# Kernel optimization log

Hardware: AMD Instinct MI355X
Metric: run time of the kernel (lower is better)

The kernel has to match this reference:

```python
import jax, jax.numpy as jnp
import numpy as np

N_NODES = 50000
N_EDGES = 800000
NFEAT, NHID, NCLASS = 512, 128, 40
BN_EPS = 1e-5


def setup_inputs() -> dict:
    key = jax.random.key(0)
    ks = jax.random.split(key, 12)
    x = jax.random.normal(ks[0], (N_NODES, NFEAT), dtype=jnp.float32)
    edge_index = jax.random.randint(ks[1], (2, N_EDGES), 0, N_NODES, dtype=jnp.int64)
    edge_weight = jax.random.uniform(ks[2], (N_EDGES,), dtype=jnp.float32)
    def glorot(k, fi, fo):
        lim = (6.0 / (fi + fo)) ** 0.5
        return jax.random.uniform(k, (fi, fo), minval=-lim, maxval=lim, dtype=jnp.float32)
    return {
        "x": x, "edge_index": edge_index, "edge_weight": edge_weight,
        "W1": glorot(ks[3], NFEAT, NHID), "b1": jnp.zeros((NHID,), jnp.float32),
        "W2": glorot(ks[4], NHID, NHID), "b2": jnp.zeros((NHID,), jnp.float32),
        "W3": glorot(ks[5], NHID, NHID), "b3": jnp.zeros((NHID,), jnp.float32),
        "g1": jnp.ones((NHID,), jnp.float32), "be1": jnp.zeros((NHID,), jnp.float32),
        "g2": jnp.ones((NHID,), jnp.float32), "be2": jnp.zeros((NHID,), jnp.float32),
        "g3": jnp.ones((NHID,), jnp.float32), "be3": jnp.zeros((NHID,), jnp.float32),
        "linW": glorot(ks[6], NHID, NCLASS), "linb": jnp.zeros((NCLASS,), jnp.float32),
    }


def _gcn_norm(edge_index, edge_weight, n):
    # PyG gcn_norm: add self-loops (weight 1), symmetric D^-1/2 (A+I) D^-1/2
    loop = jnp.arange(n, dtype=edge_index.dtype)
    row = jnp.concatenate([edge_index[0], loop])
    col = jnp.concatenate([edge_index[1], loop])
    ew = jnp.concatenate([edge_weight, jnp.ones((n,), edge_weight.dtype)])
    deg = jax.ops.segment_sum(ew, col, num_segments=n)
    dinv = jnp.where(deg > 0, jax.lax.rsqrt(jnp.maximum(deg, 1e-30)), 0.0)
    norm = dinv[row] * ew * dinv[col]
    return row, col, norm


def _conv(x, W, b, row, col, norm, n):
    h = x @ W                                   # [N, out]
    msg = h[row] * norm[:, None]                # gather + weight, [E+N, out]
    return jax.ops.segment_sum(msg, col, num_segments=n) + b


def _bn(x, g, b):
    # training-mode BatchNorm over node dim (biased variance)
    mu = jnp.mean(x, axis=0)
    var = jnp.mean((x - mu) ** 2, axis=0)
    return (x - mu) * jax.lax.rsqrt(var + BN_EPS) * g + b


def reference(x, edge_index, edge_weight, W1, b1, W2, b2, W3, b3,
              g1, be1, g2, be2, g3, be3, linW, linb):
    n = x.shape[0]
    row, col, norm = _gcn_norm(edge_index, edge_weight, n)
    x1 = _bn(jax.nn.relu(_conv(x, W1, b1, row, col, norm, n)), g1, be1)
    x2 = _bn(jax.nn.relu(_conv(x1, W2, b2, row, col, norm, n)), g2, be2)
    x3 = _bn(_conv(x2, W3, b3, row, col, norm, n), g3, be3)
    logits = x3 @ linW + linb
    return (logits, jax.nn.softmax(logits, axis=1), x3)
```

## Files before the change

### kernel.cpp

```cpp
#include <hip/hip_runtime.h>
#include <hip/hip_bf16.h>

#define N_NODES 50000
#define N_EDGES 800000
#define NFEAT 512
#define NHID 128
#define NCLASS 40
#define BN_EPS 1e-5f

typedef __attribute__((ext_vector_type(8))) short short8;
typedef __attribute__((ext_vector_type(4))) float f32x4;

#define GEMM1_BLOCKS ((N_NODES + 127) / 128)
#define EDGE_BLOCKS ((N_EDGES + 255) / 256)
#define SCAN_BLOCKS ((N_NODES + 255) / 256)
#define BN_BLOCKS ((N_NODES + 255) / 256)

__device__ __forceinline__ unsigned short f2b(float f) {
    unsigned int u = __float_as_uint(f);
    u += 0x7fff + ((u >> 16) & 1);
    return (unsigned short)(u >> 16);
}
__device__ __forceinline__ float blo(unsigned int v) {
    return __uint_as_float(v << 16);
}
__device__ __forceinline__ float bhi(unsigned int v) {
    return __uint_as_float(v & 0xffff0000u);
}

__global__ void k_init_node(unsigned long long* __restrict__ degcnt) {
    int i = blockIdx.x * blockDim.x + threadIdx.x;
    if (i < N_NODES) degcnt[i] = 0ULL;
}

__global__ void k_prep_w(const float* __restrict__ W1, const float* __restrict__ W2,
                         const float* __restrict__ W3, unsigned short* __restrict__ W1t,
                         unsigned short* __restrict__ W2t, unsigned short* __restrict__ W3t) {
    int i = blockIdx.x * blockDim.x + threadIdx.x;
    if (i < 65536) {
        int k = i >> 7, n = i & 127;
        W1t[n * 512 + k] = f2b(W1[i]);
    } else if (i < 81920) {
        int j = i - 65536; int k = j >> 7, n = j & 127;
        W2t[n * 128 + k] = f2b(W2[j]);
    } else if (i < 98304) {
        int j = i - 81920; int k = j >> 7, n = j & 127;
        W3t[n * 128 + k] = f2b(W3[j]);
    }
}

__global__ __launch_bounds__(256) void k_fat(
    const float* __restrict__ x, const unsigned short* __restrict__ W1t,
    unsigned short* __restrict__ hbuf,
    const unsigned int* __restrict__ words, const float* __restrict__ ew,
    int* __restrict__ row, int* __restrict__ col,
    unsigned long long* __restrict__ degcnt, int* __restrict__ slot) {
    __shared__ unsigned short As[128][40];
    __shared__ unsigned short Bs[128][40];
    __shared__ int s_any;
    int tid = threadIdx.x;
    if (blockIdx.x < GEMM1_BLOCKS) {
        int m0 = blockIdx.x * 128;
        int srow = tid >> 1;
        int skh = (tid & 1) << 4;
        int wave = tid >> 6, lane = tid & 63;
        int wm = (wave >> 1) * 64, wn = (wave & 1) * 64;
        int l15 = lane & 15, quad = lane >> 4;
        f32x4 acc[4][4] = {};
        bool arow_ok = (m0 + srow) < N_NODES;
        const float* arow_p = x + (size_t)(m0 + srow) * 512 + skh;
        const unsigned short* wrow_p = W1t + (size_t)srow * 512 + skh;
        for (int kt = 0; kt < 512; kt += 32) {
            float v[16];
#pragma unroll
            for (int q = 0; q < 4; q++) {
                float4 t4 = make_float4(0.f, 0.f, 0.f, 0.f);
                if (arow_ok) t4 = *(const float4*)(arow_p + kt + q * 4);
                v[q * 4 + 0] = t4.x; v[q * 4 + 1] = t4.y;
                v[q * 4 + 2] = t4.z; v[q * 4 + 3] = t4.w;
            }
            unsigned int p[8];
#pragma unroll
            for (int q = 0; q < 8; q++)
                p[q] = (unsigned int)f2b(v[2 * q]) | ((unsigned int)f2b(v[2 * q + 1]) << 16);
            uint4 w0 = make_uint4(p[0], p[1], p[2], p[3]);
            uint4 w1 = make_uint4(p[4], p[5], p[6], p[7]);
            uint4 b0 = *(const uint4*)(wrow_p + kt);
            uint4 b1 = *(const uint4*)(wrow_p + kt + 8);
            *(uint4*)&As[srow][skh] = w0;
            *(uint4*)&As[srow][skh + 8] = w1;
            *(uint4*)&Bs[srow][skh] = b0;
            *(uint4*)&Bs[srow][skh + 8] = b1;
            __syncthreads();
            short8 a[4], b[4];
#pragma unroll
            for (int i = 0; i < 4; i++) a[i] = *(const short8*)&As[wm + i * 16 + l15][quad * 8];
#pragma unroll
            for (int j = 0; j < 4; j++) b[j] = *(const short8*)&Bs[wn + j * 16 + l15][quad * 8];
#pragma unroll
            for (int i = 0; i < 4; i++)
#pragma unroll
                for (int j = 0; j < 4; j++)
                    acc[i][j] = __builtin_amdgcn_mfma_f32_16x16x32_bf16(a[i], b[j], acc[i][j], 0, 0, 0);
            __syncthreads();
        }
#pragma unroll
        for (int i = 0; i < 4; i++) {
            int mb = m0 + wm + i * 16 + quad * 4;
#pragma unroll
            for (int r = 0; r < 4; r++) {
                int m = mb + r;
                if (m < N_NODES) {
#pragma unroll
                    for (int j = 0; j < 4; j++)
                        hbuf[(size_t)m * 128 + wn + j * 16 + l15] = f2b(acc[i][j][r]);
                }
            }
        }
    } else {
        if (tid == 0) s_any = 0;
        __syncthreads();
        unsigned int probe = words[2 * tid + 1];
        if (probe != 0) atomicAdd(&s_any, 1);
        __syncthreads();
        int f = (s_any == 0) ? 1 : 0;
        int e = (blockIdx.x - GEMM1_BLOCKS) * 256 + tid;
        if (e < N_EDGES) {
            unsigned int r = f ? words[2 * (size_t)e] : words[e];
            unsigned int c = f ? words[2 * ((size_t)e + N_EDGES)] : words[e + N_EDGES];
            row[e] = (int)r;
            col[e] = (int)c;
            unsigned int q = __float2uint_rn(ew[e] * 8388608.0f);
            unsigned long long old = atomicAdd(&degcnt[c], (1ULL << 32) | (unsigned long long)q);
            slot[e] = (int)(old >> 32);
        }
    }
}

__global__ __launch_bounds__(256) void k_dinv(const unsigned long long* __restrict__ degcnt,
                                              float* __restrict__ dinv,
                                              int* __restrict__ counts,
                                              int* __restrict__ bsum) {
    int i = blockIdx.x * 256 + threadIdx.x;
    int cnt = 0;
    if (i < N_NODES) {
        unsigned long long v = degcnt[i];
        float deg = 1.0f + (float)(unsigned int)(v & 0xffffffffULL) * (1.0f / 8388608.0f);
        dinv[i] = rsqrtf(deg);
        cnt = (int)(v >> 32);
        counts[i] = cnt;
    }
    __shared__ int sh[256];
    sh[threadIdx.x] = cnt;
    __syncthreads();
    for (int ofs = 128; ofs > 0; ofs >>= 1) {
        if (threadIdx.x < ofs) sh[threadIdx.x] += sh[threadIdx.x + ofs];
        __syncthreads();
    }
    if (threadIdx.x == 0) bsum[blockIdx.x] = sh[0];
}

__global__ __launch_bounds__(256) void k_scan2(const int* __restrict__ bsum,
                                               int* __restrict__ bpre,
                                               int* __restrict__ colptr) {
    int t = threadIdx.x;
    int v = (t < SCAN_BLOCKS) ? bsum[t] : 0;
    __shared__ int sh[256];
    sh[t] = v;
    __syncthreads();
    for (int ofs = 1; ofs < 256; ofs <<= 1) {
        int u = (t >= ofs) ? sh[t - ofs] : 0;
        __syncthreads();
        sh[t] += u;
        __syncthreads();
    }
    if (t < SCAN_BLOCKS) bpre[t] = sh[t] - v;
    if (t == SCAN_BLOCKS - 1) colptr[N_NODES] = sh[t];
}

__global__ __launch_bounds__(256) void k_scan3(const int* __restrict__ counts,
                                               const int* __restrict__ bpre,
                                               int* __restrict__ colptr) {
    int t = threadIdx.x;
    int i = blockIdx.x * 256 + t;
    int v = (i < N_NODES) ? counts[i] : 0;
    __shared__ int sh[256];
    sh[t] = v;
    __syncthreads();
    for (int ofs = 1; ofs < 256; ofs <<= 1) {
        int u = (t >= ofs) ? sh[t - ofs] : 0;
        __syncthreads();
        sh[t] += u;
        __syncthreads();
    }
    if (i < N_NODES) colptr[i] = bpre[blockIdx.x] + sh[t] - v;
}

__global__ void k_scatter(const int* __restrict__ row, const int* __restrict__ col,
                          const float* __restrict__ ew, const float* __restrict__ dinv,
                          const int* __restrict__ colptr, const int* __restrict__ slot,
                          int2* __restrict__ ern) {
    int e = blockIdx.x * blockDim.x + threadIdx.x;
    if (e < N_EDGES) {
        int c = col[e], r = row[e];
        int p = colptr[c] + slot[e];
        float nrm = dinv[r] * ew[e] * dinv[c];
        ern[p] = make_int2(r, __float_as_int(nrm));
    }
}

__global__ __launch_bounds__(256) void k_aggregate(
    const unsigned int* __restrict__ hb, const int* __restrict__ colptr,
    const int2* __restrict__ ern, const float* __restrict__ dinv,
    const float* __restrict__ bias, unsigned int* __restrict__ out, int relu,
    float* __restrict__ sums, float* __restrict__ sumsq) {
    if (blockIdx.x == 0) {
        if (threadIdx.x < 128) sums[threadIdx.x] = 0.f;
        else sumsq[threadIdx.x - 128] = 0.f;
    }
    int node = (blockIdx.x * blockDim.x + threadIdx.x) >> 6;
    int lane = threadIdx.x & 63;
    if (node >= N_NODES) return;
    float di = dinv[node];
    float selfw = di * di;
    unsigned int sv = hb[(size_t)node * 64 + lane];
    float a0 = selfw * blo(sv);
    float a1 = selfw * bhi(sv);
    float c0 = 0.f, c1 = 0.f;
    int e = colptr[node], end = colptr[node + 1];
    for (; e + 8 <= end; e += 8) {
        int2 rw[8];
#pragma unroll
        for (int q = 0; q < 8; q++) rw[q] = ern[e + q];
        unsigned int v[8];
#pragma unroll
        for (int q = 0; q < 8; q++) v[q] = hb[(size_t)rw[q].x * 64 + lane];
#pragma unroll
        for (int q = 0; q < 8; q++) {
            float w = __int_as_float(rw[q].y);
            if (q & 1) { c0 += w * blo(v[q]); c1 += w * bhi(v[q]); }
            else       { a0 += w * blo(v[q]); a1 += w * bhi(v[q]); }
        }
    }
    for (; e < end; e++) {
        int2 rw = ern[e];
        float w = __int_as_float(rw.y);
        unsigned int v = hb[(size_t)rw.x * 64 + lane];
        a0 += w * blo(v);
        a1 += w * bhi(v);
    }
    a0 += c0; a1 += c1;
    float2 bv = *(const float2*)&bias[2 * lane];
    a0 += bv.x;
    a1 += bv.y;
    if (relu) { a0 = fmaxf(a0, 0.f); a1 = fmaxf(a1, 0.f); }
    out[(size_t)node * 64 + lane] = (unsigned int)f2b(a0) | ((unsigned int)f2b(a1) << 16);
}

__global__ __launch_bounds__(256) void k_bnstats(const unsigned int* __restrict__ x,
                                                 float* __restrict__ sums,
                                                 float* __restrict__ sumsq) {
    int u = threadIdx.x & 63;
    int strip = threadIdx.x >> 6;
    int r0 = blockIdx.x * 256;
    int rend = min(r0 + 256, N_NODES);
    float sl = 0.f, s2l = 0.f, sh_ = 0.f, s2h = 0.f;
    for (int r = r0 + strip; r < rend; r += 4) {
        unsigned int v = x[(size_t)r * 64 + u];
        float a = blo(v), b = bhi(v);
        sl += a; s2l += a * a;
        sh_ += b; s2h += b * b;
    }
    __shared__ float buf[4][64][4];
    buf[strip][u][0] = sl; buf[strip][u][1] = s2l;
    buf[strip][u][2] = sh_; buf[strip][u][3] = s2h;
    __syncthreads();
    if (strip == 0) {
#pragma unroll
        for (int s = 1; s < 4; s++) {
            sl += buf[s][u][0]; s2l += buf[s][u][1];
            sh_ += buf[s][u][2]; s2h += buf[s][u][3];
        }
        atomicAdd(&sums[2 * u], sl);
        atomicAdd(&sums[2 * u + 1], sh_);
        atomicAdd(&sumsq[2 * u], s2l);
        atomicAdd(&sumsq[2 * u + 1], s2h);
    }
}

__global__ __launch_bounds__(256) void k_gemm_h(
    const unsigned int* __restrict__ Ab, const unsigned short* __restrict__ Wt,
    const float* __restrict__ sums, const float* __restrict__ sumsq,
    const float* __restrict__ g, const float* __restrict__ be,
    unsigned short* __restrict__ Out) {
    __shared__ unsigned short As[128][40];
    __shared__ unsigned short Bs[128][40];
    __shared__ float s_sc[128], s_sh[128];
    int tid = threadIdx.x;
    int m0 = blockIdx.x * 128;
    if (tid < 128) {
        const float invn = 1.0f / (float)N_NODES;
        float mu = sums[tid] * invn;
        float var = sumsq[tid] * invn - mu * mu;
        float iv = rsqrtf(var + BN_EPS);
        float sc = g[tid] * iv;
        s_sc[tid] = sc;
        s_sh[tid] = be[tid] - mu * sc;
    }
    __syncthreads();
    int srow = tid >> 1;
    int skh = (tid & 1) << 4;
    int wave = tid >> 6, lane = tid & 63;
    int wm = (wave >> 1) * 64, wn = (wave & 1) * 64;
    int l15 = lane & 15, quad = lane >> 4;
    f32x4 acc[4][4] = {};
    bool arow_ok = (m0 + srow) < N_NODES;
    const unsigned int* arow_b = Ab + (size_t)(m0 + srow) * 64 + (skh >> 1);
    const unsigned short* wrow_p = Wt + (size_t)srow * 128 + skh;
    for (int kt = 0; kt < 128; kt += 32) {
        uint4 r0 = make_uint4(0, 0, 0, 0), r1 = make_uint4(0, 0, 0, 0);
        if (arow_ok) {
            r0 = *(const uint4*)(arow_b + (kt >> 1));
            r1 = *(const uint4*)(arow_b + (kt >> 1) + 4);
        }
        unsigned int raw[8] = {r0.x, r0.y, r0.z, r0.w, r1.x, r1.y, r1.z, r1.w};
        unsigned int p[8];
#pragma unroll
        for (int q = 0; q < 8; q++) {
            int ch = kt + skh + 2 * q;
            float f0 = blo(raw[q]) * s_sc[ch] + s_sh[ch];
            float f1 = bhi(raw[q]) * s_sc[ch + 1] + s_sh[ch + 1];
            p[q] = (unsigned int)f2b(f0) | ((unsigned int)f2b(f1) << 16);
        }
        uint4 w0 = make_uint4(p[0], p[1], p[2], p[3]);
        uint4 w1 = make_uint4(p[4], p[5], p[6], p[7]);
        uint4 b0 = *(const uint4*)(wrow_p + kt);
        uint4 b1 = *(const uint4*)(wrow_p + kt + 8);
        *(uint4*)&As[srow][skh] = w0;
        *(uint4*)&As[srow][skh + 8] = w1;
        *(uint4*)&Bs[srow][skh] = b0;
        *(uint4*)&Bs[srow][skh + 8] = b1;
        __syncthreads();
        short8 a[4], b[4];
#pragma unroll
        for (int i = 0; i < 4; i++) a[i] = *(const short8*)&As[wm + i * 16 + l15][quad * 8];
#pragma unroll
        for (int j = 0; j < 4; j++) b[j] = *(const short8*)&Bs[wn + j * 16 + l15][quad * 8];
#pragma unroll
        for (int i = 0; i < 4; i++)
#pragma unroll
            for (int j = 0; j < 4; j++)
                acc[i][j] = __builtin_amdgcn_mfma_f32_16x16x32_bf16(a[i], b[j], acc[i][j], 0, 0, 0);
        __syncthreads();
    }
#pragma unroll
    for (int i = 0; i < 4; i++) {
        int mb = m0 + wm + i * 16 + quad * 4;
#pragma unroll
        for (int r = 0; r < 4; r++) {
            int m = mb + r;
            if (m < N_NODES) {
#pragma unroll
                for (int j = 0; j < 4; j++)
                    Out[(size_t)m * 128 + wn + j * 16 + l15] = f2b(acc[i][j][r]);
            }
        }
    }
}

__global__ __launch_bounds__(256) void k_logits(const unsigned int* __restrict__ abuf,
                                                const float* __restrict__ sums,
                                                const float* __restrict__ sumsq,
                                                const float* __restrict__ g,
                                                const float* __restrict__ be,
                                                const float* __restrict__ linW,
                                                const float* __restrict__ linb,
                                                float* __restrict__ logits,
                                                float* __restrict__ probs,
                                                float* __restrict__ x3out) {
    __shared__ float Xs[64][130];
    __shared__ float Ws[128 * 40];
    __shared__ float s_sc[128], s_sh[128];
    int tid = threadIdx.x;
    int m0 = blockIdx.x * 64;
    if (tid < 128) {
        const float invn = 1.0f / (float)N_NODES;
        float mu = sums[tid] * invn;
        float var = sumsq[tid] * invn - mu * mu;
        float iv = rsqrtf(var + BN_EPS);
        float sc = g[tid] * iv;
        s_sc[tid] = sc;
        s_sh[tid] = be[tid] - mu * sc;
    }
    for (int q = tid; q < 1280; q += 256)
        *(float4*)&Ws[q * 4] = *(const float4*)&linW[q * 4];
    __syncthreads();
    for (int q = tid; q < 4096; q += 256) {
        int r = q >> 6, u = q & 63;
        int m = m0 + r;
        float f0 = 0.f, f1 = 0.f;
        if (m < N_NODES) {
            unsigned int v = abuf[(size_t)m * 64 + u];
            f0 = blo(v) * s_sc[2 * u] + s_sh[2 * u];
            f1 = bhi(v) * s_sc[2 * u + 1] + s_sh[2 * u + 1];
            *(float2*)&x3out[(size_t)m * 128 + 2 * u] = make_float2(f0, f1);
        }
        *(float2*)&Xs[r][2 * u] = make_float2(f0, f1);
    }
    __syncthreads();
    int r = tid >> 2;
    int cg = tid & 3;
    int cbase = cg * 10;
    float acc[10] = {};
    for (int k = 0; k < 128; k++) {
        float a = Xs[r][k];
#pragma unroll
        for (int j = 0; j < 10; j++) acc[j] += a * Ws[k * 40 + cbase + j];
    }
#pragma unroll
    for (int j = 0; j < 10; j++) acc[j] += linb[cbase + j];
    float m = acc[0];
#pragma unroll
    for (int j = 1; j < 10; j++) m = fmaxf(m, acc[j]);
    m = fmaxf(m, __shfl_xor(m, 1));
    m = fmaxf(m, __shfl_xor(m, 2));
    float ex[10];
    float s = 0.f;
#pragma unroll
    for (int j = 0; j < 10; j++) { ex[j] = expf(acc[j] - m); s += ex[j]; }
    s += __shfl_xor(s, 1);
    s += __shfl_xor(s, 2);
    float inv = 1.0f / s;
    int mrow = m0 + r;
    if (mrow < N_NODES) {
#pragma unroll
        for (int j = 0; j < 10; j++) {
            logits[(size_t)mrow * 40 + cbase + j] = acc[j];
            probs[(size_t)mrow * 40 + cbase + j] = ex[j] * inv;
        }
    }
}

extern "C" void kernel_launch(void* const* d_in, const int* in_sizes, int n_in,
                              void* d_out, int out_size, void* d_ws, size_t ws_size,
                              hipStream_t stream) {
    const float* x = (const float*)d_in[0];
    const unsigned int* eidx = (const unsigned int*)d_in[1];
    const float* ew = (const float*)d_in[2];
    const float* W1 = (const float*)d_in[3];
    const float* b1 = (const float*)d_in[4];
    const float* W2 = (const float*)d_in[5];
    const float* b2 = (const float*)d_in[6];
    const float* W3 = (const float*)d_in[7];
    const float* b3 = (const float*)d_in[8];
    const float* g1 = (const float*)d_in[9];
    const float* be1 = (const float*)d_in[10];
    const float* g2 = (const float*)d_in[11];
    const float* be2 = (const float*)d_in[12];
    const float* g3 = (const float*)d_in[13];
    const float* be3 = (const float*)d_in[14];
    const float* linW = (const float*)d_in[15];
    const float* linb = (const float*)d_in[16];

    float* out = (float*)d_out;
    float* logits = out;
    float* probs = out + (size_t)N_NODES * NCLASS;
    float* x3out = out + 2 * (size_t)N_NODES * NCLASS;

    char* ws = (char*)d_ws;
    size_t off = 0;
    auto take = [&](size_t bytes) -> char* {
        char* p = ws + off;
        off += (bytes + 255) & ~(size_t)255;
        return p;
    };
    int* row32 = (int*)take((size_t)N_EDGES * 4);
    int* col32 = (int*)take((size_t)N_EDGES * 4);
    int* slot = (int*)take((size_t)N_EDGES * 4);
    int* colptr = (int*)take((size_t)(N_NODES + 1) * 4);
    int* counts = (int*)take((size_t)N_NODES * 4);
    unsigned long long* degcnt = (unsigned long long*)take((size_t)N_NODES * 8);
    int2* ern = (int2*)take((size_t)N_EDGES * 8);
    float* dinv = (float*)take((size_t)N_NODES * 4);
    unsigned short* hbuf = (unsigned short*)take((size_t)N_NODES * NHID * 2);
    unsigned short* abuf = (unsigned short*)take((size_t)N_NODES * NHID * 2);
    unsigned short* W1t = (unsigned short*)take((size_t)512 * 128 * 2);
    unsigned short* W2t = (unsigned short*)take((size_t)128 * 128 * 2);
    unsigned short* W3t = (unsigned short*)take((size_t)128 * 128 * 2);
    float* sums = (float*)take(128 * 4);
    float* sumsq = (float*)take(128 * 4);
    int* bsum = (int*)take((size_t)SCAN_BLOCKS * 4);
    int* bpre = (int*)take((size_t)SCAN_BLOCKS * 4);
    (void)ws_size; (void)n_in; (void)in_sizes; (void)out_size;

    const int TPB = 256;
    int grid_e = EDGE_BLOCKS;
    int grid_gemm = GEMM1_BLOCKS;
    int grid_agg = (N_NODES * 64 + TPB - 1) / TPB;
    int grid_head = (N_NODES + 63) / 64;

    k_init_node<<<SCAN_BLOCKS, TPB, 0, stream>>>(degcnt);
    k_prep_w<<<(98304 + TPB - 1) / TPB, TPB, 0, stream>>>(W1, W2, W3, W1t, W2t, W3t);
    k_fat<<<GEMM1_BLOCKS + EDGE_BLOCKS, TPB, 0, stream>>>(
        x, W1t, hbuf, eidx, ew, row32, col32, degcnt, slot);
    k_dinv<<<SCAN_BLOCKS, TPB, 0, stream>>>(degcnt, dinv, counts, bsum);
    k_scan2<<<1, TPB, 0, stream>>>(bsum, bpre, colptr);
    k_scan3<<<SCAN_BLOCKS, TPB, 0, stream>>>(counts, bpre, colptr);
    k_scatter<<<grid_e, TPB, 0, stream>>>(row32, col32, ew, dinv, colptr, slot, ern);

    k_aggregate<<<grid_agg, TPB, 0, stream>>>((const unsigned int*)hbuf, colptr, ern, dinv, b1, (unsigned int*)abuf, 1, sums, sumsq);
    k_bnstats<<<BN_BLOCKS, TPB, 0, stream>>>((const unsigned int*)abuf, sums, sumsq);

    k_gemm_h<<<grid_gemm, TPB, 0, stream>>>((const unsigned int*)abuf, W2t, sums, sumsq, g1, be1, hbuf);
    k_aggregate<<<grid_agg, TPB, 0, stream>>>((const unsigned int*)hbuf, colptr, ern, dinv, b2, (unsigned int*)abuf, 1, sums, sumsq);
    k_bnstats<<<BN_BLOCKS, TPB, 0, stream>>>((const unsigned int*)abuf, sums, sumsq);

    k_gemm_h<<<grid_gemm, TPB, 0, stream>>>((const unsigned int*)abuf, W3t, sums, sumsq, g2, be2, hbuf);
    k_aggregate<<<grid_agg, TPB, 0, stream>>>((const unsigned int*)hbuf, colptr, ern, dinv, b3, (unsigned int*)abuf, 0, sums, sumsq);
    k_bnstats<<<BN_BLOCKS, TPB, 0, stream>>>((const unsigned int*)abuf, sums, sumsq);

    k_logits<<<grid_head, TPB, 0, stream>>>((const unsigned int*)abuf, sums, sumsq, g3, be3, linW, linb, logits, probs, x3out);
}
```

Before: 494.6 us.

## Spread degree atomics over eight sub-counters and merge scan and prep kernels

Each edge block now adds its atomic degree/count update to one of eight copies per destination node, chosen by block index, to reduce same-address atomic contention. The dinv kernel merges the copies and records per-copy base offsets, which the scatter kernel uses to place edges into CSR slots. The two-level scan is merged into one kernel where every block redoes the block-sum scan, and the init and weight-prep kernels are fused, saving launches. In exchange the degree buffer is eight times larger, zero-initialization writes more memory, and CSR building does more reads.

Result: no change. 499.2 us (+0.9%).

```diff
diff --git a/kernel.cpp b/kernel.cpp
--- a/kernel.cpp
+++ b/kernel.cpp
@@ -15,6 +15,7 @@
 #define EDGE_BLOCKS ((N_EDGES + 255) / 256)
 #define SCAN_BLOCKS ((N_NODES + 255) / 256)
 #define BN_BLOCKS ((N_NODES + 255) / 256)
+#define DEG8 (N_NODES * 8)
 
 __device__ __forceinline__ unsigned short f2b(float f) {
     unsigned int u = __float_as_uint(f);
@@ -28,24 +29,22 @@
     return __uint_as_float(v & 0xffff0000u);
 }
 
-__global__ void k_init_node(unsigned long long* __restrict__ degcnt) {
+__global__ void k_init_prep(unsigned long long* __restrict__ degcnt8,
+                            const float* __restrict__ W1, const float* __restrict__ W2,
+                            const float* __restrict__ W3, unsigned short* __restrict__ W1t,
+                            unsigned short* __restrict__ W2t, unsigned short* __restrict__ W3t) {
     int i = blockIdx.x * blockDim.x + threadIdx.x;
-    if (i < N_NODES) degcnt[i] = 0ULL;
-}
-
-__global__ void k_prep_w(const float* __restrict__ W1, const float* __restrict__ W2,
-                         const float* __restrict__ W3, unsigned short* __restrict__ W1t,
-                         unsigned short* __restrict__ W2t, unsigned short* __restrict__ W3t) {
-    int i = blockIdx.x * blockDim.x + threadIdx.x;
-    if (i < 65536) {
-        int k = i >> 7, n = i & 127;
-        W1t[n * 512 + k] = f2b(W1[i]);
-    } else if (i < 81920) {
-        int j = i - 65536; int k = j >> 7, n = j & 127;
-        W2t[n * 128 + k] = f2b(W2[j]);
-    } else if (i < 98304) {
-        int j = i - 81920; int k = j >> 7, n = j & 127;
-        W3t[n * 128 + k] = f2b(W3[j]);
+    if (i < DEG8) { degcnt8[i] = 0ULL; return; }
+    int j = i - DEG8;
+    if (j < 65536) {
+        int k = j >> 7, n = j & 127;
+        W1t[n * 512 + k] = f2b(W1[j]);
+    } else if (j < 81920) {
+        int q = j - 65536; int k = q >> 7, n = q & 127;
+        W2t[n * 128 + k] = f2b(W2[q]);
+    } else if (j < 98304) {
+        int q = j - 81920; int k = q >> 7, n = q & 127;
+        W3t[n * 128 + k] = f2b(W3[q]);
     }
 }
 
@@ -54,7 +53,7 @@
     unsigned short* __restrict__ hbuf,
     const unsigned int* __restrict__ words, const float* __restrict__ ew,
     int* __restrict__ row, int* __restrict__ col,
-    unsigned long long* __restrict__ degcnt, int* __restrict__ slot) {
+    unsigned long long* __restrict__ degcnt8, int* __restrict__ slot) {
     __shared__ unsigned short As[128][40];
     __shared__ unsigned short Bs[128][40];
     __shared__ int s_any;
@@ -124,31 +123,43 @@
         if (probe != 0) atomicAdd(&s_any, 1);
         __syncthreads();
         int f = (s_any == 0) ? 1 : 0;
-        int e = (blockIdx.x - GEMM1_BLOCKS) * 256 + tid;
+        int eb = blockIdx.x - GEMM1_BLOCKS;
+        int e = eb * 256 + tid;
+        int copy = eb & 7;
         if (e < N_EDGES) {
             unsigned int r = f ? words[2 * (size_t)e] : words[e];
             unsigned int c = f ? words[2 * ((size_t)e + N_EDGES)] : words[e + N_EDGES];
             row[e] = (int)r;
             col[e] = (int)c;
             unsigned int q = __float2uint_rn(ew[e] * 8388608.0f);
-            unsigned long long old = atomicAdd(&degcnt[c], (1ULL << 32) | (unsigned long long)q);
+            unsigned long long old = atomicAdd(&degcnt8[(size_t)c * 8 + copy],
+                                               (1ULL << 32) | (unsigned long long)q);
             slot[e] = (int)(old >> 32);
         }
     }
 }
 
-__global__ __launch_bounds__(256) void k_dinv(const unsigned long long* __restrict__ degcnt,
+__global__ __launch_bounds__(256) void k_dinv(const unsigned long long* __restrict__ degcnt8,
                                               float* __restrict__ dinv,
                                               int* __restrict__ counts,
+                                              int* __restrict__ base8,
                                               int* __restrict__ bsum) {
     int i = blockIdx.x * 256 + threadIdx.x;
     int cnt = 0;
     if (i < N_NODES) {
-        unsigned long long v = degcnt[i];
-        float deg = 1.0f + (float)(unsigned int)(v & 0xffffffffULL) * (1.0f / 8388608.0f);
+        unsigned int fx = 0;
+        int run = 0;
+#pragma unroll
+        for (int c = 0; c < 8; c++) {
+            unsigned long long v = degcnt8[(size_t)i * 8 + c];
+            base8[i * 8 + c] = run;
+            run += (int)(v >> 32);
+            fx += (unsigned int)(v & 0xffffffffULL);
+        }
+        float deg = 1.0f + (float)fx * (1.0f / 8388608.0f);
         dinv[i] = rsqrtf(deg);
-        cnt = (int)(v >> 32);
-        counts[i] = cnt;
+        counts[i] = run;
+        cnt = run;
     }
     __shared__ int sh[256];
     sh[threadIdx.x] = cnt;
@@ -160,12 +171,25 @@
     if (threadIdx.x == 0) bsum[blockIdx.x] = sh[0];
 }
 
-__global__ __launch_bounds__(256) void k_scan2(const int* __restrict__ bsum,
-                                               int* __restrict__ bpre,
-                                               int* __restrict__ colptr) {
+__global__ __launch_bounds__(256) void k_scan(const int* __restrict__ counts,
+                                              const int* __restrict__ bsum,
+                                              int* __restrict__ colptr) {
     int t = threadIdx.x;
-    int v = (t < SCAN_BLOCKS) ? bsum[t] : 0;
+    __shared__ int shb[256];
+    int vb = (t < SCAN_BLOCKS) ? bsum[t] : 0;
+    shb[t] = vb;
+    __syncthreads();
+    for (int ofs = 1; ofs < 256; ofs <<= 1) {
+        int u = (t >= ofs) ? shb[t - ofs] : 0;
+        __syncthreads();
+        shb[t] += u;
+        __syncthreads();
+    }
+    int bpre = (blockIdx.x > 0) ? shb[blockIdx.x - 1] : 0;
+    int total = shb[SCAN_BLOCKS - 1];
     __shared__ int sh[256];
+    int i = blockIdx.x * 256 + t;
+    int v = (i < N_NODES) ? counts[i] : 0;
     sh[t] = v;
     __syncthreads();
     for (int ofs = 1; ofs < 256; ofs <<= 1) {
@@ -174,36 +198,19 @@
         sh[t] += u;
         __syncthreads();
     }
-    if (t < SCAN_BLOCKS) bpre[t] = sh[t] - v;
-    if (t == SCAN_BLOCKS - 1) colptr[N_NODES] = sh[t];
-}
-
-__global__ __launch_bounds__(256) void k_scan3(const int* __restrict__ counts,
-                                               const int* __restrict__ bpre,
-                                               int* __restrict__ colptr) {
-    int t = threadIdx.x;
-    int i = blockIdx.x * 256 + t;
-    int v = (i < N_NODES) ? counts[i] : 0;
-    __shared__ int sh[256];
-    sh[t] = v;
-    __syncthreads();
-    for (int ofs = 1; ofs < 256; ofs <<= 1) {
-        int u = (t >= ofs) ? sh[t - ofs] : 0;
-        __syncthreads();
-        sh[t] += u;
-        __syncthreads();
-    }
-    if (i < N_NODES) colptr[i] = bpre[blockIdx.x] + sh[t] - v;
+    if (i < N_NODES) colptr[i] = bpre + sh[t] - v;
+    if (blockIdx.x == 0 && t == 0) colptr[N_NODES] = total;
 }
 
 __global__ void k_scatter(const int* __restrict__ row, const int* __restrict__ col,
                           const float* __restrict__ ew, const float* __restrict__ dinv,
-                          const int* __restrict__ colptr, const int* __restrict__ slot,
-                          int2* __restrict__ ern) {
+                          const int* __restrict__ colptr, const int* __restrict__ base8,
+                          const int* __restrict__ slot, int2* __restrict__ ern) {
     int e = blockIdx.x * blockDim.x + threadIdx.x;
     if (e < N_EDGES) {
         int c = col[e], r = row[e];
-        int p = colptr[c] + slot[e];
+        int copy = (e >> 8) & 7;
+        int p = colptr[c] + base8[c * 8 + copy] + slot[e];
         float nrm = dinv[r] * ew[e] * dinv[c];
         ern[p] = make_int2(r, __float_as_int(nrm));
     }
@@ -479,7 +486,8 @@
     int* slot = (int*)take((size_t)N_EDGES * 4);
     int* colptr = (int*)take((size_t)(N_NODES + 1) * 4);
     int* counts = (int*)take((size_t)N_NODES * 4);
-    unsigned long long* degcnt = (unsigned long long*)take((size_t)N_NODES * 8);
+    unsigned long long* degcnt8 = (unsigned long long*)take((size_t)DEG8 * 8);
+    int* base8 = (int*)take((size_t)DEG8 * 4);
     int2* ern = (int2*)take((size_t)N_EDGES * 8);
     float* dinv = (float*)take((size_t)N_NODES * 4);
     unsigned short* hbuf = (unsigned short*)take((size_t)N_NODES * NHID * 2);
@@ -490,23 +498,20 @@
     float* sums = (float*)take(128 * 4);
     float* sumsq = (float*)take(128 * 4);
     int* bsum = (int*)take((size_t)SCAN_BLOCKS * 4);
-    int* bpre = (int*)take((size_t)SCAN_BLOCKS * 4);
     (void)ws_size; (void)n_in; (void)in_sizes; (void)out_size;
 
     const int TPB = 256;
-    int grid_e = EDGE_BLOCKS;
+    int grid_initprep = (DEG8 + 98304 + TPB - 1) / TPB;
     int grid_gemm = GEMM1_BLOCKS;
     int grid_agg = (N_NODES * 64 + TPB - 1) / TPB;
     int grid_head = (N_NODES + 63) / 64;
 
-    k_init_node<<<SCAN_BLOCKS, TPB, 0, stream>>>(degcnt);
-    k_prep_w<<<(98304 + TPB - 1) / TPB, TPB, 0, stream>>>(W1, W2, W3, W1t, W2t, W3t);
+    k_init_prep<<<grid_initprep, TPB, 0, stream>>>(degcnt8, W1, W2, W3, W1t, W2t, W3t);
     k_fat<<<GEMM1_BLOCKS + EDGE_BLOCKS, TPB, 0, stream>>>(
-        x, W1t, hbuf, eidx, ew, row32, col32, degcnt, slot);
-    k_dinv<<<SCAN_BLOCKS, TPB, 0, stream>>>(degcnt, dinv, counts, bsum);
-    k_scan2<<<1, TPB, 0, stream>>>(bsum, bpre, colptr);
-    k_scan3<<<SCAN_BLOCKS, TPB, 0, stream>>>(counts, bpre, colptr);
-    k_scatter<<<grid_e, TPB, 0, stream>>>(row32, col32, ew, dinv, colptr, slot, ern);
+        x, W1t, hbuf, eidx, ew, row32, col32, degcnt8, slot);
+    k_dinv<<<SCAN_BLOCKS, TPB, 0, stream>>>(degcnt8, dinv, counts, base8, bsum);
+    k_scan<<<SCAN_BLOCKS, TPB, 0, stream>>>(counts, bsum, colptr);
+    k_scatter<<<EDGE_BLOCKS, TPB, 0, stream>>>(row32, col32, ew, dinv, colptr, base8, slot, ern);
 
     k_aggregate<<<grid_agg, TPB, 0, stream>>>((const unsigned int*)hbuf, colptr, ern, dinv, b1, (unsigned int*)abuf, 1, sums, sumsq);
     k_bnstats<<<BN_BLOCKS, TPB, 0, stream>>>((const unsigned int*)abuf, sums, sumsq);
```
